# Optimization experiments

Hardware: AMD Instinct MI355X
Metric: run time of the kernel (lower is better)

Reference implementation:

```python
import jax, jax.numpy as jnp
import numpy as np

SCALE = 480  # matches init scale_factor

def _pchip_slopes(y):
    """Fritsch-Carlson monotone cubic slopes for uniform unit spacing.
    y: [B, T] -> slopes [B, T]. Same math as scipy.interpolate.PchipInterpolator
    with h_i == 1 (t_in = arange(T))."""
    delta = y[:, 1:] - y[:, :-1]            # [B, T-1] secant slopes (h=1)
    d0, d1 = delta[:, :-1], delta[:, 1:]    # [B, T-2]
    prod = d0 * d1
    safe = jnp.where(prod > 0, d0 + d1, 1.0)
    # uniform spacing -> weighted harmonic mean reduces to plain harmonic mean
    interior = jnp.where(prod > 0, 2.0 * prod / safe, 0.0)

    def edge(dA, dB):
        # one-sided three-point estimate, h0 = h1 = 1
        d = (3.0 * dA - dB) * 0.5
        d = jnp.where(jnp.sign(d) != jnp.sign(dA), 0.0, d)
        d = jnp.where((jnp.sign(dA) != jnp.sign(dB)) & (jnp.abs(d) > 3.0 * jnp.abs(dA)),
                      3.0 * dA, d)
        return d

    left = edge(delta[:, 0], delta[:, 1])[:, None]
    right = edge(delta[:, -1], delta[:, -2])[:, None]
    return jnp.concatenate([left, interior, right], axis=1)  # [B, T]

def _pchip_upsample(x, scale):
    B, _, T = x.shape
    y = x[:, 0, :]                           # [B, T]
    d = _pchip_slopes(y)                     # [B, T]
    T_out = T * scale
    # query grid spanning the full knot range t_in = 0..T-1 (intended behavior)
    t = jnp.linspace(0.0, float(T - 1), T_out)
    idx = jnp.clip(jnp.floor(t).astype(jnp.int32), 0, T - 2)  # interval index
    s = t - idx                              # local coordinate in [0, 1]
    one_m_s = 1.0 - s
    s2 = s * s
    h00 = (1.0 + 2.0 * s) * one_m_s * one_m_s
    h10 = s * one_m_s * one_m_s
    h01 = s2 * (3.0 - 2.0 * s)
    h11 = s2 * (s - 1.0)
    # gather + cubic Hermite eval, fully vectorized over [B, T_out]
    out = (h00 * y[:, idx] + h10 * d[:, idx]
           + h01 * y[:, idx + 1] + h11 * d[:, idx + 1])
    return out[:, None, :]                   # [B, 1, T_out]

def setup_inputs() -> dict:
    key = jax.random.key(0)
    x = jax.random.normal(key, (32, 1, 2048), dtype=jnp.float32)
    return {"x": x}

def reference(x):
    return _pchip_upsample(x, SCALE)
```

## Files before the change

### kernel.cpp

```cpp
#include <hip/hip_runtime.h>

#define T_IN 2048
#define UPSCALE 480
#define T_OUT (T_IN * UPSCALE)
#define BPB 64
#define CHUNK (T_OUT / BPB)
#define NTHREADS 256
#define ITERS (CHUNK / 4 / NTHREADS)

__device__ __forceinline__ float signf(float x) {
    return (x > 0.f) ? 1.f : ((x < 0.f) ? -1.f : 0.f);
}

__device__ __forceinline__ float edge_slope(float dA, float dB) {
    float d = (3.f * dA - dB) * 0.5f;
    if (signf(d) != signf(dA)) {
        d = 0.f;
    } else if ((signf(dA) != signf(dB)) && (fabsf(d) > 3.f * fabsf(dA))) {
        d = 3.f * dA;
    }
    return d;
}

__global__ __launch_bounds__(NTHREADS) void pchip_upsample_kernel(
    const float* __restrict__ x, float* __restrict__ out)
{
    __shared__ float sy[T_IN];
    __shared__ float sd[T_IN];

    const int b   = blockIdx.y;
    const int cb  = blockIdx.x;
    const int tid = threadIdx.x;

    const float* xb = x + (size_t)b * T_IN;
    for (int i = tid; i < T_IN; i += NTHREADS) sy[i] = xb[i];
    __syncthreads();

    for (int i = tid; i < T_IN; i += NTHREADS) {
        float dv;
        if (i == 0) {
            float dA = sy[1] - sy[0];
            float dB = sy[2] - sy[1];
            dv = edge_slope(dA, dB);
        } else if (i == T_IN - 1) {
            float dA = sy[T_IN - 1] - sy[T_IN - 2];
            float dB = sy[T_IN - 2] - sy[T_IN - 3];
            dv = edge_slope(dA, dB);
        } else {
            float d0 = sy[i] - sy[i - 1];
            float d1 = sy[i + 1] - sy[i];
            float prod = d0 * d1;
            dv = (prod > 0.f) ? (2.f * prod / (d0 + d1)) : 0.f;
        }
        sd[i] = dv;
    }
    __syncthreads();

    const float STEP = (float)(T_IN - 1) / (float)(T_OUT - 1);

    float4* outv = (float4*)(out + (size_t)b * T_OUT + (size_t)cb * CHUNK);
    const int jbase = cb * CHUNK;

    for (int it = 0; it < ITERS; ++it) {
        const int g  = it * NTHREADS + tid;
        const int j0 = jbase + g * 4;
        float4 r;
        #pragma unroll
        for (int k = 0; k < 4; ++k) {
            float t = (float)(j0 + k) * STEP;
            int idx = (int)t;
            idx = idx > (T_IN - 2) ? (T_IN - 2) : idx;
            float s = t - (float)idx;

            float y0 = sy[idx],     y1 = sy[idx + 1];
            float d0 = sd[idx],     d1 = sd[idx + 1];

            float oms  = 1.f - s;
            float oms2 = oms * oms;
            float s2   = s * s;
            float h00  = (1.f + 2.f * s) * oms2;
            float h10  = s * oms2;
            float h01  = s2 * (3.f - 2.f * s);
            float h11  = s2 * (s - 1.f);

            float v = h00 * y0 + h10 * d0 + h01 * y1 + h11 * d1;
            if (k == 0) r.x = v;
            else if (k == 1) r.y = v;
            else if (k == 2) r.z = v;
            else r.w = v;
        }
        outv[g] = r;
    }
}

extern "C" void kernel_launch(void* const* d_in, const int* in_sizes, int n_in,
                              void* d_out, int out_size, void* d_ws, size_t ws_size,
                              hipStream_t stream) {
    (void)d_ws; (void)ws_size; (void)n_in; (void)out_size;
    const float* x = (const float*)d_in[0];
    float* out = (float*)d_out;
    const int B = in_sizes[0] / T_IN;

    dim3 grid(BPB, B);
    pchip_upsample_kernel<<<grid, NTHREADS, 0, stream>>>(x, out);
}
```

Baseline: 28.04 us.

## Precompute per-interval cubic polynomial coefficients and evaluate with Horner FMAs

```diff
diff --git a/kernel.cpp b/kernel.cpp
--- a/kernel.cpp
+++ b/kernel.cpp
@@ -7,6 +7,7 @@
 #define CHUNK (T_OUT / BPB)
 #define NTHREADS 256
 #define ITERS (CHUNK / 4 / NTHREADS)
+#define NINTERVAL (T_IN - 1)
 
 __device__ __forceinline__ float signf(float x) {
     return (x > 0.f) ? 1.f : ((x < 0.f) ? -1.f : 0.f);
@@ -22,11 +23,28 @@
     return d;
 }
 
+__device__ __forceinline__ float slope_at(const float* sy, int i) {
+    if (i == 0) {
+        float dA = sy[1] - sy[0];
+        float dB = sy[2] - sy[1];
+        return edge_slope(dA, dB);
+    } else if (i == T_IN - 1) {
+        float dA = sy[T_IN - 1] - sy[T_IN - 2];
+        float dB = sy[T_IN - 2] - sy[T_IN - 3];
+        return edge_slope(dA, dB);
+    } else {
+        float d0 = sy[i] - sy[i - 1];
+        float d1 = sy[i + 1] - sy[i];
+        float p = d0 * d1;
+        return (p > 0.f) ? (2.f * p / (d0 + d1)) : 0.f;
+    }
+}
+
 __global__ __launch_bounds__(NTHREADS) void pchip_upsample_kernel(
     const float* __restrict__ x, float* __restrict__ out)
 {
-    __shared__ float sy[T_IN];
-    __shared__ float sd[T_IN];
+    __shared__ float4 scoef[NINTERVAL];
+    float* sy = (float*)scoef;
 
     const int b   = blockIdx.y;
     const int cb  = blockIdx.x;
@@ -36,24 +54,26 @@
     for (int i = tid; i < T_IN; i += NTHREADS) sy[i] = xb[i];
     __syncthreads();
 
-    for (int i = tid; i < T_IN; i += NTHREADS) {
-        float dv;
-        if (i == 0) {
-            float dA = sy[1] - sy[0];
-            float dB = sy[2] - sy[1];
-            dv = edge_slope(dA, dB);
-        } else if (i == T_IN - 1) {
-            float dA = sy[T_IN - 1] - sy[T_IN - 2];
-            float dB = sy[T_IN - 2] - sy[T_IN - 3];
-            dv = edge_slope(dA, dB);
-        } else {
-            float d0 = sy[i] - sy[i - 1];
-            float d1 = sy[i + 1] - sy[i];
-            float prod = d0 * d1;
-            dv = (prod > 0.f) ? (2.f * prod / (d0 + d1)) : 0.f;
-        }
-        sd[i] = dv;
+    float4 creg[ITERS > 8 ? ITERS : 8];
+    int   cidx[8];
+    int   ncoef = 0;
+    for (int i = tid; i < NINTERVAL; i += NTHREADS) {
+        float y0 = sy[i], y1 = sy[i + 1];
+        float d0 = slope_at(sy, i);
+        float d1 = slope_at(sy, i + 1);
+        float dy = y1 - y0;
+        float4 c;
+        c.x = y0;
+        c.y = d0;
+        c.z = 3.f * dy - 2.f * d0 - d1;
+        c.w = d0 + d1 - 2.f * dy;
+        creg[ncoef] = c;
+        cidx[ncoef] = i;
+        ++ncoef;
     }
+    __syncthreads();
+
+    for (int k = 0; k < ncoef; ++k) scoef[cidx[k]] = creg[k];
     __syncthreads();
 
     const float STEP = (float)(T_IN - 1) / (float)(T_OUT - 1);
@@ -69,21 +89,10 @@
         for (int k = 0; k < 4; ++k) {
             float t = (float)(j0 + k) * STEP;
             int idx = (int)t;
-            idx = idx > (T_IN - 2) ? (T_IN - 2) : idx;
+            idx = idx > (NINTERVAL - 1) ? (NINTERVAL - 1) : idx;
             float s = t - (float)idx;
-
-            float y0 = sy[idx],     y1 = sy[idx + 1];
-            float d0 = sd[idx],     d1 = sd[idx + 1];
-
-            float oms  = 1.f - s;
-            float oms2 = oms * oms;
-            float s2   = s * s;
-            float h00  = (1.f + 2.f * s) * oms2;
-            float h10  = s * oms2;
-            float h01  = s2 * (3.f - 2.f * s);
-            float h11  = s2 * (s - 1.f);
-
-            float v = h00 * y0 + h10 * d0 + h01 * y1 + h11 * d1;
+            float4 c = scoef[idx];
+            float v = __builtin_fmaf(__builtin_fmaf(__builtin_fmaf(c.w, s, c.z), s, c.y), s, c.x);
             if (k == 0) r.x = v;
             else if (k == 1) r.y = v;
             else if (k == 2) r.z = v;
```

After: 63.08 us. +125.0%, slower.
